# Optimization experiments

Measured on AMD Instinct MI355X. Metric: run time of the kernel, lower is better.

Reference implementation:

```python
import jax, jax.numpy as jnp
import numpy as np

N, E, G = 50000, 800000, 512
F_IN, ED, NUM_CLASSES = 128, 3, 10
H1, C1, C2 = 4, 32, 64


def _add_self_loops(src, dst, eattr, n):
    # PyG add_self_loops with fill_value='mean': loop attr = mean of incoming edge attrs
    cnt = jax.ops.segment_sum(jnp.ones_like(dst, dtype=eattr.dtype), dst, num_segments=n)
    loop = jax.ops.segment_sum(eattr, dst, num_segments=n) / jnp.maximum(cnt, 1.0)[:, None]
    ar = jnp.arange(n)
    return (jnp.concatenate([src, ar]), jnp.concatenate([dst, ar]),
            jnp.concatenate([eattr, loop], axis=0))


def _gatv2(x, src, dst, eattr, Wl, bl, Wr, br, We, att, bias, heads, out_ch, concat, n):
    xl = (x @ Wl.T + bl).reshape(n, heads, out_ch)   # source transform (lin_l)
    xr = (x @ Wr.T + br).reshape(n, heads, out_ch)   # target transform (lin_r)
    ee = (eattr @ We.T).reshape(-1, heads, out_ch)   # edge transform (lin_edge, no bias)
    m = jax.nn.leaky_relu(xl[src] + xr[dst] + ee, 0.2)  # [E', H, C]
    score = jnp.einsum('ehc,hc->eh', m, att)
    # segment softmax over incoming edges of each target node
    smax = jax.ops.segment_max(score, dst, num_segments=n)
    ex = jnp.exp(score - smax[dst])
    denom = jax.ops.segment_sum(ex, dst, num_segments=n)
    alpha = ex / denom[dst]
    out = jax.ops.segment_sum(alpha[:, :, None] * xl[src], dst, num_segments=n)
    out = out.reshape(n, heads * out_ch) if concat else out.mean(axis=1)
    return out + bias


def setup_inputs() -> dict:
    key = jax.random.key(0)
    ks = jax.random.split(key, 24)
    s = 0.1
    return {
        'x': jax.random.normal(ks[0], (N, F_IN), jnp.float32),
        'edge_index': jax.random.randint(ks[1], (2, E), 0, N),
        'edge_attr': jax.random.normal(ks[2], (E, ED), jnp.float32),
        'batch': jnp.sort(jax.random.randint(ks[3], (N,), 0, G)),
        'u': jax.random.normal(ks[4], (G, 1), jnp.float32),
        'Wl1': jax.random.normal(ks[5], (H1 * C1, F_IN), jnp.float32) * s,
        'bl1': jnp.zeros((H1 * C1,), jnp.float32),
        'Wr1': jax.random.normal(ks[6], (H1 * C1, F_IN), jnp.float32) * s,
        'br1': jnp.zeros((H1 * C1,), jnp.float32),
        'We1': jax.random.normal(ks[7], (H1 * C1, ED), jnp.float32) * s,
        'att1': jax.random.normal(ks[8], (H1, C1), jnp.float32) * s,
        'b1': jnp.zeros((H1 * C1,), jnp.float32),
        'Wl2': jax.random.normal(ks[9], (C2, H1 * C1), jnp.float32) * s,
        'bl2': jnp.zeros((C2,), jnp.float32),
        'Wr2': jax.random.normal(ks[10], (C2, H1 * C1), jnp.float32) * s,
        'br2': jnp.zeros((C2,), jnp.float32),
        'We2': jax.random.normal(ks[11], (C2, ED), jnp.float32) * s,
        'att2': jax.random.normal(ks[12], (1, C2), jnp.float32) * s,
        'b2': jnp.zeros((C2,), jnp.float32),
        'W_lin1': jax.random.normal(ks[13], (32, 65), jnp.float32) * s,
        'b_lin1': jnp.zeros((32,), jnp.float32),
        'W_head': jax.random.normal(ks[14], (NUM_CLASSES, 32), jnp.float32) * s,
        'b_head': jnp.zeros((NUM_CLASSES,), jnp.float32),
    }


def reference(x, edge_index, edge_attr, batch, u,
              Wl1, bl1, Wr1, br1, We1, att1, b1,
              Wl2, bl2, Wr2, br2, We2, att2, b2,
              W_lin1, b_lin1, W_head, b_head):
    n = x.shape[0]
    src, dst, ea = _add_self_loops(edge_index[0], edge_index[1], edge_attr, n)
    h = jax.nn.elu(_gatv2(x, src, dst, ea, Wl1, bl1, Wr1, br1, We1, att1, b1, H1, C1, True, n))
    h = jax.nn.elu(_gatv2(h, src, dst, ea, Wl2, bl2, Wr2, br2, We2, att2, b2, 1, C2, False, n))
    cnt = jax.ops.segment_sum(jnp.ones((n,), h.dtype), batch, num_segments=G)
    pooled = jax.ops.segment_sum(h, batch, num_segments=G) / jnp.maximum(cnt, 1.0)[:, None]
    z = jax.nn.relu(jnp.concatenate([pooled, u], axis=1) @ W_lin1.T + b_lin1)
    return z @ W_head.T + b_head
```

## Files before the change

### kernel.cpp

```cpp
#include <hip/hip_runtime.h>
#include <hip/hip_fp16.h>
#include <math.h>


union H2U { __half2 h; unsigned u; };
typedef _Float16 hv2_t __attribute__((ext_vector_type(2)));
typedef unsigned uv4_t __attribute__((ext_vector_type(4)));
typedef _Float16 f16x8 __attribute__((ext_vector_type(8)));
typedef float f32x4 __attribute__((ext_vector_type(4)));

__device__ __forceinline__ __half2 hmax2(__half2 a, __half2 b) {
  union { __half2 h; hv2_t v; } x, y, r;
  x.h = a; y.h = b;
  r.v = __builtin_elementwise_max(x.v, y.v);
  return r.h;
}

#if __has_builtin(__builtin_amdgcn_fdot2)
__device__ __forceinline__ float dot2f(__half2 a, __half2 b, float c) {
  union { __half2 h; hv2_t v; } x, y;
  x.h = a; y.h = b;
  return __builtin_amdgcn_fdot2(x.v, y.v, c, false);
}
#else
__device__ __forceinline__ float dot2f(__half2 a, __half2 b, float c) {
  float2 af = __half22float2(a), bf = __half22float2(b);
  return fmaf(af.x, bf.x, fmaf(af.y, bf.y, c));
}
#endif

#if __has_builtin(__builtin_amdgcn_exp2f)
__device__ __forceinline__ float fexp2(float x) { return __builtin_amdgcn_exp2f(x); }
#else
__device__ __forceinline__ float fexp2(float x) { return exp2f(x); }
#endif

#if __has_builtin(__builtin_amdgcn_readlane)
__device__ __forceinline__ int rdlane(int v, int l) {
  return __builtin_amdgcn_readlane(v, l);
}
#else
__device__ __forceinline__ int rdlane(int v, int l) { return __shfl(v, l); }
#endif

#if __has_builtin(__builtin_amdgcn_update_dpp)
template <int CTRL>
__device__ __forceinline__ float dpp_add(float v) {
  int r = __builtin_amdgcn_update_dpp(0, __builtin_bit_cast(int, v),
                                      CTRL, 0xf, 0xf, true);
  return v + __builtin_bit_cast(float, r);
}
__device__ __forceinline__ float row_sum16(float v) {
  v = dpp_add<0x121>(v);
  v = dpp_add<0x122>(v);
  v = dpp_add<0x124>(v);
  v = dpp_add<0x128>(v);
  return v;
}
#else
__device__ __forceinline__ float row_sum16(float v) {
  v += __shfl_xor(v, 1);
  v += __shfl_xor(v, 2);
  v += __shfl_xor(v, 4);
  v += __shfl_xor(v, 8);
  return v;
}
#endif

__device__ __forceinline__ float lowf(unsigned u) {
  H2U t; t.u = u;
  return __half2float(__low2half(t.h));
}

#define LOG2E 1.44269504088896f

__global__ void hist_k(const int* __restrict__ dst, int* __restrict__ deg,
                       int* __restrict__ rank, int E) {
  int e = blockIdx.x * 256 + threadIdx.x;
  if (e < E) rank[e] = atomicAdd(&deg[dst[e]], 1);
}

__global__ void blocksum_k(const int* __restrict__ deg, int* __restrict__ bsum, int N) {
  __shared__ int s[256];
  int i = blockIdx.x * 256 + threadIdx.x;
  s[threadIdx.x] = (i < N) ? deg[i] : 0;
  __syncthreads();
  for (int off = 128; off; off >>= 1) {
    if (threadIdx.x < off) s[threadIdx.x] += s[threadIdx.x + off];
    __syncthreads();
  }
  if (threadIdx.x == 0) bsum[blockIdx.x] = s[0];
}

__global__ void writeptr_k(const int* __restrict__ deg, const int* __restrict__ bsum,
                           int* __restrict__ rowptr, int N, int E) {
  __shared__ int s[256];
  __shared__ int bs[256];
  int t = threadIdx.x;
  int i = blockIdx.x * 256 + t;
  bs[t] = (t < (int)blockIdx.x) ? bsum[t] : 0;
  s[t] = (i < N) ? deg[i] : 0;
  __syncthreads();
  for (int off = 128; off; off >>= 1) {
    if (t < off) bs[t] += bs[t + off];
    __syncthreads();
  }
  int base = bs[0];
  __syncthreads();
  for (int off = 1; off < 256; off <<= 1) {
    int v = (t >= off) ? s[t - off] : 0;
    __syncthreads();
    if (t >= off) s[t] += v;
    __syncthreads();
  }
  int excl = base + ((t == 0) ? 0 : s[t - 1]) + i;
  if (i < N) rowptr[i] = excl;
  if (i == N - 1) rowptr[N] = E + N;
}

__global__ void fill_k(const int* __restrict__ src, const int* __restrict__ dst,
                       const float* __restrict__ eattr, const int* __restrict__ rowptr,
                       const int* __restrict__ rank, uint4* __restrict__ erec, int E) {
  int e = blockIdx.x * 256 + threadIdx.x;
  if (e >= E) return;
  int pos = rowptr[dst[e]] + rank[e];
  H2U a0, a1, a2;
  float e0 = eattr[e * 3 + 0], e1 = eattr[e * 3 + 1], e2 = eattr[e * 3 + 2];
  a0.h = __floats2half2_rn(e0, e0);
  a1.h = __floats2half2_rn(e1, e1);
  a2.h = __floats2half2_rn(e2, e2);
  uv4_t v = {(unsigned)src[e], a0.u, a1.u, a2.u};
  __builtin_nontemporal_store(v, (uv4_t*)&erec[pos]);
}

__global__ void loopattr_k(const int* __restrict__ rowptr, uint4* __restrict__ erec, int N) {
  int lane = threadIdx.x & 63;
  int n = (int)((blockIdx.x * 256 + threadIdx.x) >> 6);
  if (n >= N) return;
  int beg = rowptr[n], endr = rowptr[n + 1] - 1;
  float f0 = 0.f, f1 = 0.f, f2 = 0.f;
  for (int i = beg + lane; i < endr; i += 64) {
    uint4 r = erec[i];
    f0 += lowf(r.y);
    f1 += lowf(r.z);
    f2 += lowf(r.w);
  }
#pragma unroll
  for (int off = 1; off < 64; off <<= 1) {
    f0 += __shfl_xor(f0, off);
    f1 += __shfl_xor(f1, off);
    f2 += __shfl_xor(f2, off);
  }
  if (lane == 0) {
    float inv = 1.0f / fmaxf((float)(endr - beg), 1.0f);
    H2U a0, a1, a2;
    a0.h = __floats2half2_rn(f0 * inv, f0 * inv);
    a1.h = __floats2half2_rn(f1 * inv, f1 * inv);
    a2.h = __floats2half2_rn(f2 * inv, f2 * inv);
    erec[endr] = make_uint4((unsigned)n, a0.u, a1.u, a2.u);
  }
}

__global__ void cvt_f32_f16_k(const float* __restrict__ src, __half* __restrict__ dst,
                              int n8) {
  int i = blockIdx.x * 256 + threadIdx.x;
  if (i >= n8) return;
  const float4* s = (const float4*)(src + (size_t)i * 8);
  float4 v0 = s[0], v1 = s[1];
  H2U h0, h1, h2, h3;
  h0.h = __floats2half2_rn(v0.x, v0.y);
  h1.h = __floats2half2_rn(v0.z, v0.w);
  h2.h = __floats2half2_rn(v1.x, v1.y);
  h3.h = __floats2half2_rn(v1.z, v1.w);
  uv4_t o = {h0.u, h1.u, h2.u, h3.u};
  *(uv4_t*)(dst + (size_t)i * 8) = o;
}

__global__ void cvt_w_all_k(const float* __restrict__ Wl1, const float* __restrict__ Wr1,
                            const float* __restrict__ Wl2, const float* __restrict__ Wr2,
                            __half* __restrict__ wh1, __half* __restrict__ wh2) {
  int i = blockIdx.x * 256 + threadIdx.x;
  if (i >= 6144) return;
  const float* s;
  __half* d;
  int off;
  if (i < 2048)      { s = Wl1; d = wh1;         off = i; }
  else if (i < 4096) { s = Wr1; d = wh1 + 16384; off = i - 2048; }
  else if (i < 5120) { s = Wl2; d = wh2;         off = i - 4096; }
  else               { s = Wr2; d = wh2 + 8192;  off = i - 5120; }
  const float4* sp = (const float4*)(s + (size_t)off * 8);
  float4 v0 = sp[0], v1 = sp[1];
  H2U h0, h1, h2, h3;
  h0.h = __floats2half2_rn(v0.x, v0.y);
  h1.h = __floats2half2_rn(v0.z, v0.w);
  h2.h = __floats2half2_rn(v1.x, v1.y);
  h3.h = __floats2half2_rn(v1.z, v1.w);
  uv4_t o = {h0.u, h1.u, h2.u, h3.u};
  *(uv4_t*)(d + (size_t)off * 8) = o;
}

template <int J>
__global__ __launch_bounds__(256) void mfma_linear2_k(
    const __half* __restrict__ Xh, const __half* __restrict__ Wh,
    const float* __restrict__ b1v, const float* __restrict__ b2v,
    __half* __restrict__ out1, __half* __restrict__ out2, int N) {
  constexpr int CG = (2 * J) / 64;
  int lane = threadIdx.x & 63;
  int wid = __builtin_amdgcn_readfirstlane(
      (int)((blockIdx.x * 256 + threadIdx.x) >> 6));
  int rt = wid / CG;
  int cg = wid - rt * CG;
  int r0 = rt * 32;
  if (r0 >= N) return;

  int koff = (lane >> 4) * 8;
  int row0 = r0 + (lane & 15);
  int row1 = row0 + 16;
  int cr0 = min(row0, N - 1), cr1 = min(row1, N - 1);

  const __half* xp0 = Xh + (size_t)cr0 * 128 + koff;
  const __half* xp1 = Xh + (size_t)cr1 * 128 + koff;
  f16x8 a0[4], a1[4];
#pragma unroll
  for (int ks = 0; ks < 4; ++ks) {
    a0[ks] = *(const f16x8*)(xp0 + ks * 32);
    a1[ks] = *(const f16x8*)(xp1 + ks * 32);
  }

  bool isT1 = (cg * 64) < J;
  const float* bt = isT1 ? b1v : b2v;
  __half* op = isT1 ? out1 : out2;
  int cbase = cg * 64 - (isT1 ? 0 : J);
  int cl = cbase + (lane & 15);
  int rA = r0 + ((lane >> 4) << 2);

#pragma unroll
  for (int ct = 0; ct < 4; ++ct) {
    int col = cg * 64 + ct * 16 + (lane & 15);
    const __half* wp = Wh + (size_t)col * 128 + koff;
    f16x8 b0 = *(const f16x8*)(wp);
    f16x8 b1_ = *(const f16x8*)(wp + 32);
    f16x8 b2_ = *(const f16x8*)(wp + 64);
    f16x8 b3_ = *(const f16x8*)(wp + 96);
    f32x4 acc0 = {0.f, 0.f, 0.f, 0.f};
    f32x4 acc1 = {0.f, 0.f, 0.f, 0.f};
    acc0 = __builtin_amdgcn_mfma_f32_16x16x32_f16(a0[0], b0, acc0, 0, 0, 0);
    acc1 = __builtin_amdgcn_mfma_f32_16x16x32_f16(a1[0], b0, acc1, 0, 0, 0);
    acc0 = __builtin_amdgcn_mfma_f32_16x16x32_f16(a0[1], b1_, acc0, 0, 0, 0);
    acc1 = __builtin_amdgcn_mfma_f32_16x16x32_f16(a1[1], b1_, acc1, 0, 0, 0);
    acc0 = __builtin_amdgcn_mfma_f32_16x16x32_f16(a0[2], b2_, acc0, 0, 0, 0);
    acc1 = __builtin_amdgcn_mfma_f32_16x16x32_f16(a1[2], b2_, acc1, 0, 0, 0);
    acc0 = __builtin_amdgcn_mfma_f32_16x16x32_f16(a0[3], b3_, acc0, 0, 0, 0);
    acc1 = __builtin_amdgcn_mfma_f32_16x16x32_f16(a1[3], b3_, acc1, 0, 0, 0);

    int cc = cl + ct * 16;
    float bb = bt[cc];
#pragma unroll
    for (int q = 0; q < 4; ++q) {
      int r = rA + q;
      if (r < N) op[(size_t)r * J + cc] = __float2half(acc0[q] + bb);
      int r2 = r + 16;
      if (r2 < N) op[(size_t)r2 * J + cc] = __float2half(acc1[q] + bb);
    }
  }
}

__global__ __launch_bounds__(128) void gat1_fused_k(
    const int* __restrict__ rowptr, const uint4* __restrict__ erec,
    const __half* __restrict__ xlh, const __half* __restrict__ xrh,
    const float* __restrict__ We, const float* __restrict__ att,
    const float* __restrict__ bias, __half* __restrict__ out, int N) {
  constexpr int CH = 8;
  int lane = threadIdx.x & 63;
  int wave = __builtin_amdgcn_readfirstlane(
      (int)((blockIdx.x * blockDim.x + threadIdx.x) >> 6));
  int n0 = wave * 2;
  if (n0 >= N) return;
  int n1 = n0 + 1;
  bool has1 = n1 < N;

  const __half2* xl2p = (const __half2*)xlh;
  const __half2* xr2p = (const __half2*)xrh;
  __half2* outp = (__half2*)out;
  int c0 = 2 * lane;
  __half2 w0p = __floats2half2_rn(We[c0 * 3 + 0], We[c0 * 3 + 3]);
  __half2 w1p = __floats2half2_rn(We[c0 * 3 + 1], We[c0 * 3 + 4]);
  __half2 w2p = __floats2half2_rn(We[c0 * 3 + 2], We[c0 * 3 + 5]);
  __half2 attp = __floats2half2_rn(att[c0] * LOG2E, att[c0 + 1] * LOG2E);
  __half2 k02 = __floats2half2_rn(0.2f, 0.2f);
  float2 bv = make_float2(bias[c0], bias[c0 + 1]);

  int b0 = rowptr[n0];
  int e0 = rowptr[n0 + 1];
  int e1 = has1 ? rowptr[n0 + 2] : e0;
  __half2 xrp0 = xr2p[(size_t)n0 * 64 + lane];
  __half2 xrp1 = xr2p[(size_t)(has1 ? n1 : n0) * 64 + lane];
  uint4 rec0 = erec[min(b0 + lane, e0 - 1)];
  uint4 rec1 = erec[min(e0 + lane, e1 - 1)];

  auto process = [&](int n, int beg, int end, __half2 xrp, uint4 myrec) {
    float acc0 = 0.f, acc1 = 0.f, den = 0.f;
    int base = beg;
    for (;;) {
      int m = min(64, end - base);
      int ncht = (m + CH - 1) / CH;
      __half2 rA[CH], rB[CH];

      auto gatherc = [&](int cidx, __half2* r) {
        int j0 = cidx * CH;
#pragma unroll
        for (int j = 0; j < CH; ++j) {
          int s = rdlane((int)myrec.x, min(j0 + j, m - 1));
          r[j] = xl2p[(size_t)s * 64 + lane];
        }
      };
      auto compc = [&](int cidx, const __half2* r) {
        int j0 = cidx * CH;
        int lim = m - j0;
#pragma unroll
        for (int j = 0; j < CH; ++j) {
          if (j < lim) {
            H2U ea0, ea1, ea2;
            ea0.u = (unsigned)rdlane((int)myrec.y, j0 + j);
            ea1.u = (unsigned)rdlane((int)myrec.z, j0 + j);
            ea2.u = (unsigned)rdlane((int)myrec.w, j0 + j);
            __half2 mm = __hadd2(r[j], xrp);
            mm = __hfma2(ea0.h, w0p, mm);
            mm = __hfma2(ea1.h, w1p, mm);
            mm = __hfma2(ea2.h, w2p, mm);
            mm = hmax2(mm, __hmul2(mm, k02));
            float v = row_sum16(dot2f(mm, attp, 0.f));
            float ex = fexp2(v);
            float2 rfF = __half22float2(r[j]);
            den += ex;
            acc0 = fmaf(ex, rfF.x, acc0);
            acc1 = fmaf(ex, rfF.y, acc1);
          }
        }
      };

      gatherc(0, rA);
      int ch = 0;
      for (; ch + 2 <= ncht; ch += 2) {
        gatherc(ch + 1, rB);
        compc(ch, rA);
        if (ch + 2 < ncht) gatherc(ch + 2, rA);
        compc(ch + 1, rB);
      }
      if (ch < ncht) compc(ch, rA);

      base += m;
      if (base >= end) break;
      myrec = erec[min(base + lane, end - 1)];
    }

    float o0 = acc0 / den + bv.x;
    float o1 = acc1 / den + bv.y;
    o0 = o0 > 0.f ? o0 : __expf(o0) - 1.0f;
    o1 = o1 > 0.f ? o1 : __expf(o1) - 1.0f;
    H2U o;
    o.h = __floats2half2_rn(o0, o1);
    outp[(size_t)n * 64 + lane] = o.h;
  };

  process(n0, b0, e0, xrp0, rec0);
  if (has1) process(n1, e0, e1, xrp1, rec1);
}

__global__ __launch_bounds__(128) void gat2_fused_k(
    const int* __restrict__ rowptr, const uint4* __restrict__ erec,
    const __half* __restrict__ xlh, const __half* __restrict__ xrh,
    const float* __restrict__ We, const float* __restrict__ att,
    const float* __restrict__ bias, float* __restrict__ out, int N) {
  constexpr int CP = 4;
  int lane = threadIdx.x & 63;
  int wave0 = __builtin_amdgcn_readfirstlane(
      (int)((blockIdx.x * blockDim.x + threadIdx.x) >> 6));
  int nwaves = (gridDim.x * blockDim.x) >> 6;
  int sub = lane & 31, grp = lane >> 5;
  int c0 = 2 * sub;
  const __half2* xl2p = (const __half2*)xlh;
  const __half2* xr2p = (const __half2*)xrh;
  __half2 w0p = __floats2half2_rn(We[c0 * 3 + 0], We[c0 * 3 + 3]);
  __half2 w1p = __floats2half2_rn(We[c0 * 3 + 1], We[c0 * 3 + 4]);
  __half2 w2p = __floats2half2_rn(We[c0 * 3 + 2], We[c0 * 3 + 5]);
  __half2 attp = __floats2half2_rn(att[c0] * LOG2E, att[c0 + 1] * LOG2E);
  __half2 k02 = __floats2half2_rn(0.2f, 0.2f);
  float2 bv = make_float2(bias[c0], bias[c0 + 1]);

  for (int n = wave0; n < N; n += nwaves) {
    __half2 xrp = xr2p[(size_t)n * 32 + sub];
    int beg = rowptr[n], end = rowptr[n + 1];
    int cnt = end - beg;

    float acc0 = 0.f, acc1 = 0.f, den = 0.f;

    int nfull = cnt / (2 * CP);
    int b = beg + grp;
    for (int ch = 0; ch < nfull; ++ch) {
      uint4 recs[CP];
      __half2 r_[CP];
#pragma unroll
      for (int j = 0; j < CP; ++j) recs[j] = erec[b + 2 * j];
#pragma unroll
      for (int j = 0; j < CP; ++j) r_[j] = xl2p[(size_t)recs[j].x * 32 + sub];
#pragma unroll
      for (int j = 0; j < CP; ++j) {
        H2U e0, e1, e2;
        e0.u = recs[j].y; e1.u = recs[j].z; e2.u = recs[j].w;
        __half2 m = __hadd2(r_[j], xrp);
        m = __hfma2(e0.h, w0p, m);
        m = __hfma2(e1.h, w1p, m);
        m = __hfma2(e2.h, w2p, m);
        m = hmax2(m, __hmul2(m, k02));
        float v = row_sum16(dot2f(m, attp, 0.f));
        v += __shfl_xor(v, 16);
        float ex = fexp2(v);
        float2 rfF = __half22float2(r_[j]);
        den += ex;
        acc0 = fmaf(ex, rfF.x, acc0);
        acc1 = fmaf(ex, rfF.y, acc1);
      }
      b += 2 * CP;
    }
    for (int gi = beg + nfull * 2 * CP + grp; gi < end; gi += 2) {
      uint4 rec = erec[gi];
      __half2 rf = xl2p[(size_t)rec.x * 32 + sub];
      H2U e0, e1, e2;
      e0.u = rec.y; e1.u = rec.z; e2.u = rec.w;
      __half2 m = __hadd2(rf, xrp);
      m = __hfma2(e0.h, w0p, m);
      m = __hfma2(e1.h, w1p, m);
      m = __hfma2(e2.h, w2p, m);
      m = hmax2(m, __hmul2(m, k02));
      float v = row_sum16(dot2f(m, attp, 0.f));
      v += __shfl_xor(v, 16);
      float ex = fexp2(v);
      float2 rfF = __half22float2(rf);
      den += ex;
      acc0 = fmaf(ex, rfF.x, acc0);
      acc1 = fmaf(ex, rfF.y, acc1);
    }

    acc0 += __shfl_xor(acc0, 32);
    acc1 += __shfl_xor(acc1, 32);
    den += __shfl_xor(den, 32);

    if (grp == 0) {
      float o0 = acc0 / den + bv.x;
      float o1 = acc1 / den + bv.y;
      o0 = o0 > 0.f ? o0 : __expf(o0) - 1.0f;
      o1 = o1 > 0.f ? o1 : __expf(o1) - 1.0f;
      *(float2*)&out[(size_t)n * 64 + c0] = make_float2(o0, o1);
    }
  }
}

__global__ void final_mlp_k(const float* __restrict__ h2, const int* __restrict__ batch,
                            int N, const float* __restrict__ u,
                            const float* __restrict__ W1, const float* __restrict__ b1,
                            const float* __restrict__ Wh, const float* __restrict__ bh,
                            float* __restrict__ out) {
  __shared__ float comb[4][64];
  __shared__ float feat[65];
  __shared__ float z[32];
  int g = blockIdx.x;
  int t = threadIdx.x;
  int c = t & 63, q = t >> 6;
  int lo, hi;
  {
    int l = 0, h = N;
    while (l < h) { int m = (l + h) >> 1; if (batch[m] < g) l = m + 1; else h = m; }
    lo = l;
    h = N;
    while (l < h) { int m = (l + h) >> 1; if (batch[m] < g + 1) l = m + 1; else h = m; }
    hi = l;
  }
  float a = 0.f;
  for (int nn = lo + q; nn < hi; nn += 4) a += h2[(size_t)nn * 64 + c];
  comb[q][c] = a;
  __syncthreads();
  if (t < 64) {
    float s = comb[0][t] + comb[1][t] + comb[2][t] + comb[3][t];
    float inv = 1.0f / fmaxf((float)(hi - lo), 1.0f);
    feat[t] = s * inv;
    if (t == 0) feat[64] = u[g];
  }
  __syncthreads();
  if (t < 32) {
    float s = b1[t];
    for (int k = 0; k < 65; ++k) s += feat[k] * W1[t * 65 + k];
    z[t] = fmaxf(s, 0.0f);
  }
  __syncthreads();
  if (t < 10) {
    float s = bh[t];
    for (int k = 0; k < 32; ++k) s += z[k] * Wh[t * 32 + k];
    out[g * 10 + t] = s;
  }
}

extern "C" void kernel_launch(void* const* d_in, const int* in_sizes, int n_in,
                              void* d_out, int out_size, void* d_ws, size_t ws_size,
                              hipStream_t stream) {
  const float* x      = (const float*)d_in[0];
  const int*   eidx   = (const int*)d_in[1];
  const float* eattr  = (const float*)d_in[2];
  const int*   batch  = (const int*)d_in[3];
  const float* u      = (const float*)d_in[4];
  const float* Wl1    = (const float*)d_in[5];
  const float* bl1    = (const float*)d_in[6];
  const float* Wr1    = (const float*)d_in[7];
  const float* br1    = (const float*)d_in[8];
  const float* We1    = (const float*)d_in[9];
  const float* att1   = (const float*)d_in[10];
  const float* b1     = (const float*)d_in[11];
  const float* Wl2    = (const float*)d_in[12];
  const float* bl2    = (const float*)d_in[13];
  const float* Wr2    = (const float*)d_in[14];
  const float* br2    = (const float*)d_in[15];
  const float* We2    = (const float*)d_in[16];
  const float* att2   = (const float*)d_in[17];
  const float* b2     = (const float*)d_in[18];
  const float* W_lin1 = (const float*)d_in[19];
  const float* b_lin1 = (const float*)d_in[20];
  const float* W_head = (const float*)d_in[21];
  const float* b_head = (const float*)d_in[22];

  const int N = in_sizes[0] / 128;
  const int E = in_sizes[1] / 2;
  const int G = in_sizes[4];
  const int* srcp = eidx;
  const int* dstp = eidx + E;

  __half* bufh = (__half*)d_ws;
  __half* bufr = bufh + (size_t)N * 128;
  float* buf3 = (float*)(bufr + (size_t)N * 128);
  __half* g1h = (__half*)buf3;
  float* h2f = (float*)(g1h + (size_t)N * 128);
  uint4* erec = (uint4*)(buf3 + (size_t)N * 128);
  __half* xh  = (__half*)erec;
  int* rank   = (int*)(erec + ((size_t)E + N));
  int* deg    = rank + E;
  int* rowptr = deg + N;
  int* bsum   = rowptr + N + 1;
  uintptr_t wtop = ((uintptr_t)(bsum + 256) + 15) & ~(uintptr_t)15;
  __half* wh1 = (__half*)wtop;
  __half* wh2 = wh1 + 32768;

  const int nb = (N + 255) / 256;
  const int gat_blocks = (N + 1) / 2;
  const int gat1_blocks = (((N + 1) / 2) + 1) / 2;
  const int rt = (N + 31) / 32;

  cvt_w_all_k<<<24, 256, 0, stream>>>(Wl1, Wr1, Wl2, Wr2, wh1, wh2);
  cvt_f32_f16_k<<<(N * 16 + 255) / 256, 256, 0, stream>>>(x, xh, N * 16);
  mfma_linear2_k<128><<<rt, 256, 0, stream>>>(xh, wh1, bl1, br1, bufh, bufr, N);

  (void)hipMemsetAsync(deg, 0, sizeof(int) * (size_t)N, stream);
  hist_k<<<(E + 255) / 256, 256, 0, stream>>>(dstp, deg, rank, E);
  blocksum_k<<<nb, 256, 0, stream>>>(deg, bsum, N);
  writeptr_k<<<nb, 256, 0, stream>>>(deg, bsum, rowptr, N, E);
  fill_k<<<(E + 255) / 256, 256, 0, stream>>>(srcp, dstp, eattr, rowptr, rank, erec, E);
  loopattr_k<<<(N * 64 + 255) / 256, 256, 0, stream>>>(rowptr, erec, N);

  gat1_fused_k<<<gat1_blocks, 128, 0, stream>>>(rowptr, erec, bufh, bufr,
                                                We1, att1, b1, g1h, N);

  mfma_linear2_k<64><<<(rt * 2 + 3) / 4, 256, 0, stream>>>(g1h, wh2, bl2, br2,
                                                           bufh, bufr, N);
  gat2_fused_k<<<gat_blocks, 128, 0, stream>>>(rowptr, erec, bufh, bufr,
                                               We2, att2, b2, h2f, N);

  final_mlp_k<<<G, 256, 0, stream>>>(h2f, batch, N, u, W_lin1, b_lin1, W_head, b_head,
                                     (float*)d_out);
}
```

Before: 350.8 us.

## Process multiple edges per wave with 4-channel lanes in both GATv2 kernels

Both fused GATv2 aggregation kernels now give each lane 4 channels (one 8-byte gather) instead of 2. Layer 1 splits the wave into two 32-lane groups that each handle an edge. Layer 2 splits it into four 16-lane groups, each on its own edge. The attention-score reduction shrinks to an 8-lane or 16-lane DPP/swizzle sum, and partial softmax accumulators are combined across groups with shuffles at the end. Layer 1 drops its readlane-broadcast chunked pipeline in favour of per-group direct record loads, and switches to one node per wave with a grid-stride loop. The aim is to raise memory-level parallelism and lower per-edge cross-lane work, in exchange for extra cross-group reductions and masked tail iterations.

```diff
diff --git a/kernel.cpp b/kernel.cpp
--- a/kernel.cpp
+++ b/kernel.cpp
@@ -33,14 +33,6 @@
 __device__ __forceinline__ float fexp2(float x) { return __builtin_amdgcn_exp2f(x); }
 #else
 __device__ __forceinline__ float fexp2(float x) { return exp2f(x); }
-#endif
-
-#if __has_builtin(__builtin_amdgcn_readlane)
-__device__ __forceinline__ int rdlane(int v, int l) {
-  return __builtin_amdgcn_readlane(v, l);
-}
-#else
-__device__ __forceinline__ int rdlane(int v, int l) { return __shfl(v, l); }
 #endif
 
 #if __has_builtin(__builtin_amdgcn_update_dpp)
@@ -56,6 +48,16 @@
   v = dpp_add<0x124>(v);
   v = dpp_add<0x128>(v);
   return v;
+}
+__device__ __forceinline__ float row_sum8(float v) {
+  v = dpp_add<0xB1>(v);
+  v = dpp_add<0x4E>(v);
+#if __has_builtin(__builtin_amdgcn_ds_swizzle)
+  int sw = __builtin_amdgcn_ds_swizzle(__builtin_bit_cast(int, v), 0x101F);
+  return v + __builtin_bit_cast(float, sw);
+#else
+  return v + __shfl_xor(v, 4);
+#endif
 }
 #else
 __device__ __forceinline__ float row_sum16(float v) {
@@ -65,11 +67,21 @@
   v += __shfl_xor(v, 8);
   return v;
 }
+__device__ __forceinline__ float row_sum8(float v) {
+  v += __shfl_xor(v, 1);
+  v += __shfl_xor(v, 2);
+  v += __shfl_xor(v, 4);
+  return v;
+}
 #endif
 
 __device__ __forceinline__ float lowf(unsigned u) {
   H2U t; t.u = u;
   return __half2float(__low2half(t.h));
+}
+
+__device__ __forceinline__ float eluf(float x) {
+  return x > 0.f ? x : __expf(x) - 1.0f;
 }
 
 #define LOG2E 1.44269504088896f
@@ -270,101 +282,95 @@
     const __half* __restrict__ xlh, const __half* __restrict__ xrh,
     const float* __restrict__ We, const float* __restrict__ att,
     const float* __restrict__ bias, __half* __restrict__ out, int N) {
-  constexpr int CH = 8;
   int lane = threadIdx.x & 63;
-  int wave = __builtin_amdgcn_readfirstlane(
+  int sub = lane & 31, grp = lane >> 5;
+  int wave0 = __builtin_amdgcn_readfirstlane(
       (int)((blockIdx.x * blockDim.x + threadIdx.x) >> 6));
-  int n0 = wave * 2;
-  if (n0 >= N) return;
-  int n1 = n0 + 1;
-  bool has1 = n1 < N;
-
-  const __half2* xl2p = (const __half2*)xlh;
-  const __half2* xr2p = (const __half2*)xrh;
-  __half2* outp = (__half2*)out;
-  int c0 = 2 * lane;
-  __half2 w0p = __floats2half2_rn(We[c0 * 3 + 0], We[c0 * 3 + 3]);
-  __half2 w1p = __floats2half2_rn(We[c0 * 3 + 1], We[c0 * 3 + 4]);
-  __half2 w2p = __floats2half2_rn(We[c0 * 3 + 2], We[c0 * 3 + 5]);
-  __half2 attp = __floats2half2_rn(att[c0] * LOG2E, att[c0 + 1] * LOG2E);
+  int nwaves = (gridDim.x * blockDim.x) >> 6;
+  int c4 = sub * 4;
+
+  __half2 w0A = __floats2half2_rn(We[(c4 + 0) * 3 + 0], We[(c4 + 1) * 3 + 0]);
+  __half2 w0B = __floats2half2_rn(We[(c4 + 2) * 3 + 0], We[(c4 + 3) * 3 + 0]);
+  __half2 w1A = __floats2half2_rn(We[(c4 + 0) * 3 + 1], We[(c4 + 1) * 3 + 1]);
+  __half2 w1B = __floats2half2_rn(We[(c4 + 2) * 3 + 1], We[(c4 + 3) * 3 + 1]);
+  __half2 w2A = __floats2half2_rn(We[(c4 + 0) * 3 + 2], We[(c4 + 1) * 3 + 2]);
+  __half2 w2B = __floats2half2_rn(We[(c4 + 2) * 3 + 2], We[(c4 + 3) * 3 + 2]);
+  __half2 attA = __floats2half2_rn(att[c4 + 0] * LOG2E, att[c4 + 1] * LOG2E);
+  __half2 attB = __floats2half2_rn(att[c4 + 2] * LOG2E, att[c4 + 3] * LOG2E);
   __half2 k02 = __floats2half2_rn(0.2f, 0.2f);
-  float2 bv = make_float2(bias[c0], bias[c0 + 1]);
-
-  int b0 = rowptr[n0];
-  int e0 = rowptr[n0 + 1];
-  int e1 = has1 ? rowptr[n0 + 2] : e0;
-  __half2 xrp0 = xr2p[(size_t)n0 * 64 + lane];
-  __half2 xrp1 = xr2p[(size_t)(has1 ? n1 : n0) * 64 + lane];
-  uint4 rec0 = erec[min(b0 + lane, e0 - 1)];
-  uint4 rec1 = erec[min(e0 + lane, e1 - 1)];
-
-  auto process = [&](int n, int beg, int end, __half2 xrp, uint4 myrec) {
-    float acc0 = 0.f, acc1 = 0.f, den = 0.f;
-    int base = beg;
-    for (;;) {
-      int m = min(64, end - base);
-      int ncht = (m + CH - 1) / CH;
-      __half2 rA[CH], rB[CH];
-
-      auto gatherc = [&](int cidx, __half2* r) {
-        int j0 = cidx * CH;
-#pragma unroll
-        for (int j = 0; j < CH; ++j) {
-          int s = rdlane((int)myrec.x, min(j0 + j, m - 1));
-          r[j] = xl2p[(size_t)s * 64 + lane];
-        }
-      };
-      auto compc = [&](int cidx, const __half2* r) {
-        int j0 = cidx * CH;
-        int lim = m - j0;
-#pragma unroll
-        for (int j = 0; j < CH; ++j) {
-          if (j < lim) {
-            H2U ea0, ea1, ea2;
-            ea0.u = (unsigned)rdlane((int)myrec.y, j0 + j);
-            ea1.u = (unsigned)rdlane((int)myrec.z, j0 + j);
-            ea2.u = (unsigned)rdlane((int)myrec.w, j0 + j);
-            __half2 mm = __hadd2(r[j], xrp);
-            mm = __hfma2(ea0.h, w0p, mm);
-            mm = __hfma2(ea1.h, w1p, mm);
-            mm = __hfma2(ea2.h, w2p, mm);
-            mm = hmax2(mm, __hmul2(mm, k02));
-            float v = row_sum16(dot2f(mm, attp, 0.f));
-            float ex = fexp2(v);
-            float2 rfF = __half22float2(r[j]);
-            den += ex;
-            acc0 = fmaf(ex, rfF.x, acc0);
-            acc1 = fmaf(ex, rfF.y, acc1);
-          }
-        }
-      };
-
-      gatherc(0, rA);
-      int ch = 0;
-      for (; ch + 2 <= ncht; ch += 2) {
-        gatherc(ch + 1, rB);
-        compc(ch, rA);
-        if (ch + 2 < ncht) gatherc(ch + 2, rA);
-        compc(ch + 1, rB);
-      }
-      if (ch < ncht) compc(ch, rA);
-
-      base += m;
-      if (base >= end) break;
-      myrec = erec[min(base + lane, end - 1)];
-    }
-
-    float o0 = acc0 / den + bv.x;
-    float o1 = acc1 / den + bv.y;
-    o0 = o0 > 0.f ? o0 : __expf(o0) - 1.0f;
-    o1 = o1 > 0.f ? o1 : __expf(o1) - 1.0f;
-    H2U o;
-    o.h = __floats2half2_rn(o0, o1);
-    outp[(size_t)n * 64 + lane] = o.h;
-  };
-
-  process(n0, b0, e0, xrp0, rec0);
-  if (has1) process(n1, e0, e1, xrp1, rec1);
+  float4 bvv = make_float4(bias[c4], bias[c4 + 1], bias[c4 + 2], bias[c4 + 3]);
+
+  for (int n = wave0; n < N; n += nwaves) {
+    uint2 xu = *(const uint2*)&xrh[(size_t)n * 128 + c4];
+    H2U xrA, xrB;
+    xrA.u = xu.x; xrB.u = xu.y;
+    int beg = rowptr[n], end = rowptr[n + 1];
+    int cnt = end - beg;
+    float a0 = 0.f, a1 = 0.f, a2 = 0.f, a3 = 0.f, den = 0.f;
+
+    auto edge2 = [&](const uint4& rec, uint2 gu, bool valid) {
+      H2U e0, e1, e2, gA, gB;
+      e0.u = rec.y; e1.u = rec.z; e2.u = rec.w;
+      gA.u = gu.x; gB.u = gu.y;
+      __half2 tA = __hfma2(e2.h, w2A, xrA.h);
+      tA = __hfma2(e1.h, w1A, tA);
+      tA = __hfma2(e0.h, w0A, tA);
+      __half2 mA = __hadd2(gA.h, tA);
+      mA = hmax2(mA, __hmul2(mA, k02));
+      __half2 tB = __hfma2(e2.h, w2B, xrB.h);
+      tB = __hfma2(e1.h, w1B, tB);
+      tB = __hfma2(e0.h, w0B, tB);
+      __half2 mB = __hadd2(gB.h, tB);
+      mB = hmax2(mB, __hmul2(mB, k02));
+      float v = dot2f(mB, attB, dot2f(mA, attA, 0.f));
+      v = row_sum8(v);
+      float ex = valid ? fexp2(v) : 0.f;
+      float2 fA = __half22float2(gA.h), fB = __half22float2(gB.h);
+      den += ex;
+      a0 = fmaf(ex, fA.x, a0);
+      a1 = fmaf(ex, fA.y, a1);
+      a2 = fmaf(ex, fB.x, a2);
+      a3 = fmaf(ex, fB.y, a3);
+    };
+
+    int nch = cnt >> 3;
+    for (int ch = 0; ch < nch; ++ch) {
+      int b = beg + ch * 8 + grp;
+      uint4 rec[4];
+      uint2 gu[4];
+#pragma unroll
+      for (int j = 0; j < 4; ++j) rec[j] = erec[b + 2 * j];
+#pragma unroll
+      for (int j = 0; j < 4; ++j)
+        gu[j] = *(const uint2*)(xlh + (size_t)rec[j].x * 128 + c4);
+#pragma unroll
+      for (int j = 0; j < 4; ++j) edge2(rec[j], gu[j], true);
+    }
+    for (int gi = beg + nch * 8; gi < end; gi += 2) {
+      int idx = gi + grp;
+      bool valid = idx < end;
+      uint4 rec = erec[valid ? idx : (end - 1)];
+      uint2 gu = *(const uint2*)(xlh + (size_t)rec.x * 128 + c4);
+      edge2(rec, gu, valid);
+    }
+
+    a0 += __shfl_xor(a0, 32);
+    a1 += __shfl_xor(a1, 32);
+    a2 += __shfl_xor(a2, 32);
+    a3 += __shfl_xor(a3, 32);
+    den += __shfl_xor(den, 32);
+
+    if (grp == 0) {
+      float o0 = eluf(a0 / den + bvv.x);
+      float o1 = eluf(a1 / den + bvv.y);
+      float o2 = eluf(a2 / den + bvv.z);
+      float o3 = eluf(a3 / den + bvv.w);
+      H2U p0, p1;
+      p0.h = __floats2half2_rn(o0, o1);
+      p1.h = __floats2half2_rn(o2, o3);
+      *(uint2*)&out[(size_t)n * 128 + c4] = make_uint2(p0.u, p1.u);
+    }
+  }
 }
 
 __global__ __launch_bounds__(128) void gat2_fused_k(
@@ -372,86 +378,91 @@
     const __half* __restrict__ xlh, const __half* __restrict__ xrh,
     const float* __restrict__ We, const float* __restrict__ att,
     const float* __restrict__ bias, float* __restrict__ out, int N) {
-  constexpr int CP = 4;
   int lane = threadIdx.x & 63;
+  int s16 = lane & 15, qr = lane >> 4;
   int wave0 = __builtin_amdgcn_readfirstlane(
       (int)((blockIdx.x * blockDim.x + threadIdx.x) >> 6));
   int nwaves = (gridDim.x * blockDim.x) >> 6;
-  int sub = lane & 31, grp = lane >> 5;
-  int c0 = 2 * sub;
-  const __half2* xl2p = (const __half2*)xlh;
-  const __half2* xr2p = (const __half2*)xrh;
-  __half2 w0p = __floats2half2_rn(We[c0 * 3 + 0], We[c0 * 3 + 3]);
-  __half2 w1p = __floats2half2_rn(We[c0 * 3 + 1], We[c0 * 3 + 4]);
-  __half2 w2p = __floats2half2_rn(We[c0 * 3 + 2], We[c0 * 3 + 5]);
-  __half2 attp = __floats2half2_rn(att[c0] * LOG2E, att[c0 + 1] * LOG2E);
+  int c4 = s16 * 4;
+
+  __half2 w0A = __floats2half2_rn(We[(c4 + 0) * 3 + 0], We[(c4 + 1) * 3 + 0]);
+  __half2 w0B = __floats2half2_rn(We[(c4 + 2) * 3 + 0], We[(c4 + 3) * 3 + 0]);
+  __half2 w1A = __floats2half2_rn(We[(c4 + 0) * 3 + 1], We[(c4 + 1) * 3 + 1]);
+  __half2 w1B = __floats2half2_rn(We[(c4 + 2) * 3 + 1], We[(c4 + 3) * 3 + 1]);
+  __half2 w2A = __floats2half2_rn(We[(c4 + 0) * 3 + 2], We[(c4 + 1) * 3 + 2]);
+  __half2 w2B = __floats2half2_rn(We[(c4 + 2) * 3 + 2], We[(c4 + 3) * 3 + 2]);
+  __half2 attA = __floats2half2_rn(att[c4 + 0] * LOG2E, att[c4 + 1] * LOG2E);
+  __half2 attB = __floats2half2_rn(att[c4 + 2] * LOG2E, att[c4 + 3] * LOG2E);
   __half2 k02 = __floats2half2_rn(0.2f, 0.2f);
-  float2 bv = make_float2(bias[c0], bias[c0 + 1]);
+  float4 bvv = make_float4(bias[c4], bias[c4 + 1], bias[c4 + 2], bias[c4 + 3]);
 
   for (int n = wave0; n < N; n += nwaves) {
-    __half2 xrp = xr2p[(size_t)n * 32 + sub];
+    uint2 xu = *(const uint2*)&xrh[(size_t)n * 64 + c4];
+    H2U xrA, xrB;
+    xrA.u = xu.x; xrB.u = xu.y;
     int beg = rowptr[n], end = rowptr[n + 1];
     int cnt = end - beg;
-
-    float acc0 = 0.f, acc1 = 0.f, den = 0.f;
-
-    int nfull = cnt / (2 * CP);
-    int b = beg + grp;
-    for (int ch = 0; ch < nfull; ++ch) {
-      uint4 recs[CP];
-      __half2 r_[CP];
-#pragma unroll
-      for (int j = 0; j < CP; ++j) recs[j] = erec[b + 2 * j];
-#pragma unroll
-      for (int j = 0; j < CP; ++j) r_[j] = xl2p[(size_t)recs[j].x * 32 + sub];
-#pragma unroll
-      for (int j = 0; j < CP; ++j) {
-        H2U e0, e1, e2;
-        e0.u = recs[j].y; e1.u = recs[j].z; e2.u = recs[j].w;
-        __half2 m = __hadd2(r_[j], xrp);
-        m = __hfma2(e0.h, w0p, m);
-        m = __hfma2(e1.h, w1p, m);
-        m = __hfma2(e2.h, w2p, m);
-        m = hmax2(m, __hmul2(m, k02));
-        float v = row_sum16(dot2f(m, attp, 0.f));
-        v += __shfl_xor(v, 16);
-        float ex = fexp2(v);
-        float2 rfF = __half22float2(r_[j]);
-        den += ex;
-        acc0 = fmaf(ex, rfF.x, acc0);
-        acc1 = fmaf(ex, rfF.y, acc1);
-      }
-      b += 2 * CP;
-    }
-    for (int gi = beg + nfull * 2 * CP + grp; gi < end; gi += 2) {
-      uint4 rec = erec[gi];
-      __half2 rf = xl2p[(size_t)rec.x * 32 + sub];
-      H2U e0, e1, e2;
+    float a0 = 0.f, a1 = 0.f, a2 = 0.f, a3 = 0.f, den = 0.f;
+
+    auto edge4 = [&](const uint4& rec, uint2 gu, bool valid) {
+      H2U e0, e1, e2, gA, gB;
       e0.u = rec.y; e1.u = rec.z; e2.u = rec.w;
-      __half2 m = __hadd2(rf, xrp);
-      m = __hfma2(e0.h, w0p, m);
-      m = __hfma2(e1.h, w1p, m);
-      m = __hfma2(e2.h, w2p, m);
-      m = hmax2(m, __hmul2(m, k02));
-      float v = row_sum16(dot2f(m, attp, 0.f));
-      v += __shfl_xor(v, 16);
-      float ex = fexp2(v);
-      float2 rfF = __half22float2(rf);
+      gA.u = gu.x; gB.u = gu.y;
+      __half2 tA = __hfma2(e2.h, w2A, xrA.h);
+      tA = __hfma2(e1.h, w1A, tA);
+      tA = __hfma2(e0.h, w0A, tA);
+      __half2 mA = __hadd2(gA.h, tA);
+      mA = hmax2(mA, __hmul2(mA, k02));
+      __half2 tB = __hfma2(e2.h, w2B, xrB.h);
+      tB = __hfma2(e1.h, w1B, tB);
+      tB = __hfma2(e0.h, w0B, tB);
+      __half2 mB = __hadd2(gB.h, tB);
+      mB = hmax2(mB, __hmul2(mB, k02));
+      float v = dot2f(mB, attB, dot2f(mA, attA, 0.f));
+      v = row_sum16(v);
+      float ex = valid ? fexp2(v) : 0.f;
+      float2 fA = __half22float2(gA.h), fB = __half22float2(gB.h);
       den += ex;
-      acc0 = fmaf(ex, rfF.x, acc0);
-      acc1 = fmaf(ex, rfF.y, acc1);
-    }
-
-    acc0 += __shfl_xor(acc0, 32);
-    acc1 += __shfl_xor(acc1, 32);
-    den += __shfl_xor(den, 32);
-
-    if (grp == 0) {
-      float o0 = acc0 / den + bv.x;
-      float o1 = acc1 / den + bv.y;
-      o0 = o0 > 0.f ? o0 : __expf(o0) - 1.0f;
-      o1 = o1 > 0.f ? o1 : __expf(o1) - 1.0f;
-      *(float2*)&out[(size_t)n * 64 + c0] = make_float2(o0, o1);
+      a0 = fmaf(ex, fA.x, a0);
+      a1 = fmaf(ex, fA.y, a1);
+      a2 = fmaf(ex, fB.x, a2);
+      a3 = fmaf(ex, fB.y, a3);
+    };
+
+    int nch = cnt >> 3;
+    for (int ch = 0; ch < nch; ++ch) {
+      int b = beg + ch * 8 + qr;
+      uint4 rec[2];
+      uint2 gu[2];
+#pragma unroll
+      for (int j = 0; j < 2; ++j) rec[j] = erec[b + 4 * j];
+#pragma unroll
+      for (int j = 0; j < 2; ++j)
+        gu[j] = *(const uint2*)(xlh + (size_t)rec[j].x * 64 + c4);
+#pragma unroll
+      for (int j = 0; j < 2; ++j) edge4(rec[j], gu[j], true);
+    }
+    for (int gi = beg + nch * 8; gi < end; gi += 4) {
+      int idx = gi + qr;
+      bool valid = idx < end;
+      uint4 rec = erec[valid ? idx : (end - 1)];
+      uint2 gu = *(const uint2*)(xlh + (size_t)rec.x * 64 + c4);
+      edge4(rec, gu, valid);
+    }
+
+    a0 += __shfl_xor(a0, 16); a0 += __shfl_xor(a0, 32);
+    a1 += __shfl_xor(a1, 16); a1 += __shfl_xor(a1, 32);
+    a2 += __shfl_xor(a2, 16); a2 += __shfl_xor(a2, 32);
+    a3 += __shfl_xor(a3, 16); a3 += __shfl_xor(a3, 32);
+    den += __shfl_xor(den, 16); den += __shfl_xor(den, 32);
+
+    if (lane < 16) {
+      float4 o;
+      o.x = eluf(a0 / den + bvv.x);
+      o.y = eluf(a1 / den + bvv.y);
+      o.z = eluf(a2 / den + bvv.z);
+      o.w = eluf(a3 / den + bvv.w);
+      *(float4*)&out[(size_t)n * 64 + c4] = o;
     }
   }
 }
@@ -550,7 +561,6 @@
 
   const int nb = (N + 255) / 256;
   const int gat_blocks = (N + 1) / 2;
-  const int gat1_blocks = (((N + 1) / 2) + 1) / 2;
   const int rt = (N + 31) / 32;
 
   cvt_w_all_k<<<24, 256, 0, stream>>>(Wl1, Wr1, Wl2, Wr2, wh1, wh2);
@@ -564,8 +574,8 @@
   fill_k<<<(E + 255) / 256, 256, 0, stream>>>(srcp, dstp, eattr, rowptr, rank, erec, E);
   loopattr_k<<<(N * 64 + 255) / 256, 256, 0, stream>>>(rowptr, erec, N);
 
-  gat1_fused_k<<<gat1_blocks, 128, 0, stream>>>(rowptr, erec, bufh, bufr,
-                                                We1, att1, b1, g1h, N);
+  gat1_fused_k<<<gat_blocks, 128, 0, stream>>>(rowptr, erec, bufh, bufr,
+                                               We1, att1, b1, g1h, N);
 
   mfma_linear2_k<64><<<(rt * 2 + 3) / 4, 256, 0, stream>>>(g1h, wh2, bl2, br2,
                                                            bufh, bufr, N);
```

New measurement: 338.1 us. 1.04x faster.
